# Kernel tuning notes

Hardware: AMD Instinct MI355X
Metric: run time of the kernel (lower is better)

Reference implementation:

```python
import jax, jax.numpy as jnp
import numpy as np

DG = 4      # deformable groups
KS = 3      # kernel size
PAD = (KS - 1) // 2


def _deform_conv2d(x, offset, weight, dg=DG, pad=PAD):
    """Deformable conv v1 (stride 1, dilation 1, same padding, no bias).
    x:      [B, Cin, H, W]
    offset: [B, dg*2*K, H, W], layout (g, k, {y,x}) in channel dim
    weight: [Cout, Cin, kh, kw]
    """
    B, Cin, H, W = x.shape
    Cout, _, kh, kw = weight.shape
    K = kh * kw
    Cg = Cin // dg
    off = offset.reshape(B, dg, K, 2, H, W)
    # kernel tap coordinates, flattened row-major
    ky = jnp.repeat(jnp.arange(kh), kw).astype(x.dtype)   # [K]
    kx = jnp.tile(jnp.arange(kw), kh).astype(x.dtype)     # [K]
    # sampling positions [B, dg, K, H, W]
    py = off[:, :, :, 0] + (jnp.arange(H, dtype=x.dtype)[None, None, None, :, None]
                            + ky[None, None, :, None, None] - pad)
    px = off[:, :, :, 1] + (jnp.arange(W, dtype=x.dtype)[None, None, None, None, :]
                            + kx[None, None, :, None, None] - pad)
    y0 = jnp.floor(py)
    x0 = jnp.floor(px)
    xg = x.reshape(B, dg, Cg, H * W)
    val = jnp.zeros((B, dg, Cg, K, H, W), x.dtype)
    for dy in (0.0, 1.0):
        for dx in (0.0, 1.0):
            yc = y0 + dy
            xc = x0 + dx
            w = (1.0 - jnp.abs(py - yc)) * (1.0 - jnp.abs(px - xc))
            valid = (yc >= 0) & (yc <= H - 1) & (xc >= 0) & (xc <= W - 1)
            w = jnp.where(valid, w, 0.0)                      # zero padding
            idx = (jnp.clip(yc, 0, H - 1).astype(jnp.int32) * W
                   + jnp.clip(xc, 0, W - 1).astype(jnp.int32))  # [B,dg,K,H,W]
            idx_b = jnp.broadcast_to(idx.reshape(B, dg, 1, K * H * W),
                                     (B, dg, Cg, K * H * W))
            g = jnp.take_along_axis(xg, idx_b, axis=3).reshape(B, dg, Cg, K, H, W)
            val = val + w[:, :, None] * g
    # grouped-offset but dense conv: contract over (dg, Cg, K)
    wk = weight.reshape(Cout, dg, Cg, K)
    return jnp.einsum('bgckhw,ogck->bohw', val, wk)


def setup_inputs() -> dict:
    key = jax.random.key(0)
    k1, k2, k3, k4, k5, k6 = jax.random.split(key, 6)
    B, C, H, W = 2, 256, 64, 64
    reg_feat = jax.random.normal(k1, (B, C, H, W), jnp.float32)
    cls_feat = jax.random.normal(k2, (B, C, H, W), jnp.float32)
    pred_init = jax.random.normal(k3, (B, 34, H, W), jnp.float32)
    w_offset = jax.random.normal(k4, (DG * 2 * KS * KS, 34), jnp.float32) * 0.1
    w_reg = jax.random.normal(k5, (C, C, KS, KS), jnp.float32) * 0.01
    w_cls = jax.random.normal(k6, (C, C, KS, KS), jnp.float32) * 0.01
    return {"reg_feat": reg_feat, "cls_feat": cls_feat, "pred_init": pred_init,
            "w_offset": w_offset, "w_reg": w_reg, "w_cls": w_cls}


def reference(reg_feat, cls_feat, pred_init, w_offset, w_reg, w_cls):
    # 1x1 conv (bias-free) predicting offsets from detached anchor predictions
    offset = jnp.einsum('oc,bchw->bohw', w_offset, jax.lax.stop_gradient(pred_init))
    reg_refine = jax.nn.relu(_deform_conv2d(reg_feat, offset, w_reg))
    cls_refine = jax.nn.relu(_deform_conv2d(cls_feat, offset, w_cls))
    return (reg_refine, cls_refine)
```

## Files before the change

kernel.cpp:

```cpp
#include <hip/hip_runtime.h>
#include <hip/hip_bf16.h>
#include <stdint.h>

#define HW   4096
#define NB   2

typedef float f32x4 __attribute__((ext_vector_type(4)));
typedef short s16x8 __attribute__((ext_vector_type(8)));

__device__ __forceinline__ unsigned short f2bf(float f) {
    union { float f; unsigned int u; } v; v.f = f;
    unsigned int u = v.u;
    unsigned int r = (u + 0x7FFFu + ((u >> 16) & 1u)) >> 16;
    return (unsigned short)r;
}

__device__ __forceinline__ float bf2f(unsigned short u) {
    union { unsigned int u; float f; } v; v.u = ((unsigned int)u) << 16;
    return v.f;
}

__global__ void __launch_bounds__(256)
k_prep(const float* __restrict__ pred, const float* __restrict__ wo,
       const float* __restrict__ regf, const float* __restrict__ clsf,
       const float* __restrict__ wr,   const float* __restrict__ wc,
       float4* __restrict__ wbuf, int4* __restrict__ ibuf,
       unsigned short* __restrict__ fbuf, unsigned short* __restrict__ wfrag) {
    int bb = blockIdx.x;
    if (bb < 1152) {
        int loc = bb * 256 + threadIdx.x;
        int p  = loc & 4095;
        int g  = (loc >> 12) & 3;
        int bk = loc >> 14;
        int b  = bk / 9;
        int k  = bk - b * 9;
        int rowy = ((g * 9 + k) * 2) * 34;
        float oy = 0.f, ox = 0.f;
        const float* pb = pred + (size_t)b * 34 * HW + p;
        #pragma unroll
        for (int c = 0; c < 34; ++c) {
            float pv = pb[c * HW];
            oy += wo[rowy + c]      * pv;
            ox += wo[rowy + 34 + c] * pv;
        }
        int h = p >> 6, w = p & 63;
        int ky = k / 3, kx = k - ky * 3;
        float py = oy + (float)(h + ky - 1);
        float px = ox + (float)(w + kx - 1);
        float fy0 = floorf(py), fx0 = floorf(px);
        int y0 = (int)fy0, x0 = (int)fx0;
        float fy = py - fy0, fx = px - fx0;
        float wy0 = 1.f - fy, wy1 = fy, wx0 = 1.f - fx, wx1 = fx;
        if (!(y0 >= 0  && y0 <= 63)) wy0 = 0.f;
        if (!(y0 >= -1 && y0 <= 62)) wy1 = 0.f;
        if (!(x0 >= 0  && x0 <= 63)) wx0 = 0.f;
        if (!(x0 >= -1 && x0 <= 62)) wx1 = 0.f;
        int cy0 = min(max(y0, 0), 63),     cy1 = min(max(y0 + 1, 0), 63);
        int cx0 = min(max(x0, 0), 63),     cx1 = min(max(x0 + 1, 0), 63);
        wbuf[loc] = make_float4(wy0 * wx0, wy0 * wx1, wy1 * wx0, wy1 * wx1);
        ibuf[loc] = make_int4((cy0 * 64 + cx0) << 9, (cy0 * 64 + cx1) << 9,
                              (cy1 * 64 + cx0) << 9, (cy1 * 64 + cx1) << 9);
    } else if (bb < 2176) {
        __shared__ float tile[64][65];
        int bid = bb - 1152;
        int pt = bid & 63;
        int cb = (bid >> 6) & 3;
        int b  = (bid >> 8) & 1;
        int cv = bid >> 9;
        const float* src = cv ? clsf : regf;
        int t = threadIdx.x;
        int pl = t & 63, q = t >> 6;
        #pragma unroll
        for (int i = 0; i < 16; ++i) {
            int cl = q + i * 4;
            tile[cl][pl] = src[((size_t)(b * 256 + cb * 64 + cl)) * HW + pt * 64 + pl];
        }
        __syncthreads();
        int cpair = t & 31, prow = t >> 5;
        #pragma unroll
        for (int i = 0; i < 8; ++i) {
            int p = i * 8 + prow;
            unsigned int u0 = f2bf(tile[cpair * 2][p]);
            unsigned int u1 = f2bf(tile[cpair * 2 + 1][p]);
            *(unsigned int*)&fbuf[((size_t)((cv * 2 + b) * HW + pt * 64 + p)) * 256
                                  + cb * 64 + cpair * 2] = u0 | (u1 << 16);
        }
    } else {
        int L = (bb - 2176) * 256 + threadIdx.x;
        int conv = L / 73728;
        int r = L - conv * 73728;
        int lane = r & 63;
        int ot = (r >> 6) & 15;
        int kk = (r >> 10) & 1;
        int s  = r >> 11;
        int k = s >> 2, g = s & 3;
        int o  = ot * 16 + (lane & 15);
        int cb = kk * 32 + (lane >> 4) * 8;
        const float* w = conv ? wc : wr;
        s16x8 v;
        #pragma unroll
        for (int j = 0; j < 8; ++j) {
            int c = cb + j;
            v[j] = (short)f2bf(w[((size_t)o * 256 + g * 64 + c) * 9 + k]);
        }
        *(s16x8*)(wfrag + (size_t)L * 8) = v;
    }
}

__global__ void __launch_bounds__(512, 2)
k_main(const float4* __restrict__ wbuf, const int4* __restrict__ ibuf,
       const unsigned short* __restrict__ fbuf, const unsigned short* __restrict__ wfrag,
       float* __restrict__ out) {
    __shared__ __align__(16) unsigned short vt[2][64][72];

    int bid0 = blockIdx.x;
    int bid = (bid0 & 7) * 32 + (bid0 >> 3);
    int conv = bid >> 7;
    int b    = (bid >> 6) & 1;
    int pt   = bid & 63;
    int p0   = pt * 64;

    int tid  = threadIdx.x;
    int lane = tid & 63;
    int wv   = tid >> 6;
    int px   = tid >> 3;
    int cg   = tid & 7;

    const char* fbb = (const char*)(fbuf + (size_t)(conv * 2 + b) * HW * 256);
    const unsigned short* wfc = wfrag + (size_t)conv * 73728 * 8;

    f32x4 acc[2][4];
    #pragma unroll
    for (int i = 0; i < 2; ++i)
        #pragma unroll
        for (int j = 0; j < 4; ++j)
            acc[i][j] = (f32x4){0.f, 0.f, 0.f, 0.f};

    struct Par { float4 w4; int4 io; };
    struct Gat { s16x8 a, b, c, d; };

    auto ldpar = [&](int s) -> Par {
        int k = s >> 2, g = s & 3;
        int pidx = ((b * 9 + k) * 4 + g) * HW + p0 + px;
        Par P; P.w4 = wbuf[pidx]; P.io = ibuf[pidx];
        return P;
    };

    auto gather = [&](const Par& P, int g) -> Gat {
        const char* base = fbb + g * 128 + cg * 16;
        Gat G;
        G.a = *(const s16x8*)(base + P.io.x);
        G.b = *(const s16x8*)(base + P.io.y);
        G.c = *(const s16x8*)(base + P.io.z);
        G.d = *(const s16x8*)(base + P.io.w);
        return G;
    };

    auto finish = [&](const Par& P, const Gat& G, int buf) {
        float r[8];
        #pragma unroll
        for (int j = 0; j < 8; ++j) {
            r[j] = P.w4.x * bf2f((unsigned short)G.a[j])
                 + P.w4.y * bf2f((unsigned short)G.b[j])
                 + P.w4.z * bf2f((unsigned short)G.c[j])
                 + P.w4.w * bf2f((unsigned short)G.d[j]);
        }
        s16x8 pk;
        #pragma unroll
        for (int j = 0; j < 8; ++j) pk[j] = (short)f2bf(r[j]);
        *(s16x8*)&vt[buf][px][cg * 8] = pk;
    };

    s16x8 af00, af01, af10, af11;
    auto loadA = [&](int s) {
        const unsigned short* wfs = wfc + (size_t)s * 2048 * 8;
        af00 = *(const s16x8*)(wfs + ((size_t)( 0 + wv * 2 + 0) * 64 + lane) * 8);
        af01 = *(const s16x8*)(wfs + ((size_t)( 0 + wv * 2 + 1) * 64 + lane) * 8);
        af10 = *(const s16x8*)(wfs + ((size_t)(16 + wv * 2 + 0) * 64 + lane) * 8);
        af11 = *(const s16x8*)(wfs + ((size_t)(16 + wv * 2 + 1) * 64 + lane) * 8);
    };

    auto domfma = [&](int s) {
        s16x8 bfr[4];
        #pragma unroll
        for (int np = 0; np < 4; ++np)
            bfr[np] = *(const s16x8*)
                &vt[s & 1][np * 16 + (lane & 15)][(lane >> 4) * 8];
        #pragma unroll
        for (int np = 0; np < 4; ++np)
            acc[0][np] = __builtin_amdgcn_mfma_f32_16x16x32_bf16(af00, bfr[np],
                                                                 acc[0][np], 0, 0, 0);
        #pragma unroll
        for (int np = 0; np < 4; ++np)
            acc[1][np] = __builtin_amdgcn_mfma_f32_16x16x32_bf16(af01, bfr[np],
                                                                 acc[1][np], 0, 0, 0);
        #pragma unroll
        for (int np = 0; np < 4; ++np)
            bfr[np] = *(const s16x8*)
                &vt[s & 1][np * 16 + (lane & 15)][32 + (lane >> 4) * 8];
        #pragma unroll
        for (int np = 0; np < 4; ++np)
            acc[0][np] = __builtin_amdgcn_mfma_f32_16x16x32_bf16(af10, bfr[np],
                                                                 acc[0][np], 0, 0, 0);
        #pragma unroll
        for (int np = 0; np < 4; ++np)
            acc[1][np] = __builtin_amdgcn_mfma_f32_16x16x32_bf16(af11, bfr[np],
                                                                 acc[1][np], 0, 0, 0);
    };

    loadA(0);
    Par P0 = ldpar(0);
    Gat G0 = gather(P0, 0);
    finish(P0, G0, 0);
    Par P1 = ldpar(1);
    Par P2 = ldpar(2);
    Gat G1 = gather(P1, 1);

    for (int s = 0; s < 36; ++s) {
        Gat Gn;
        Par Pn;
        if (s + 2 < 36) Gn = gather(P2, (s + 2) & 3);
        Pn = (s + 3 < 36) ? ldpar(s + 3) : P2;
        asm volatile("s_waitcnt lgkmcnt(0)" ::: "memory");
        __builtin_amdgcn_s_barrier();
        domfma(s);
        if (s + 1 < 36) {
            loadA(s + 1);
            finish(P1, G1, (s + 1) & 1);
        }
        P1 = P2; P2 = Pn; G1 = Gn;
    }

    float* ob = out + (size_t)conv * (NB * 256 * HW) + (size_t)b * 256 * HW;
    #pragma unroll
    for (int mo = 0; mo < 2; ++mo)
        #pragma unroll
        for (int np = 0; np < 4; ++np)
            #pragma unroll
            for (int r = 0; r < 4; ++r) {
                int o = wv * 32 + mo * 16 + (lane >> 4) * 4 + r;
                int p = p0 + np * 16 + (lane & 15);
                float v = acc[mo][np][r];
                ob[(size_t)o * HW + p] = v > 0.f ? v : 0.f;
            }
}

extern "C" void kernel_launch(void* const* d_in, const int* in_sizes, int n_in,
                              void* d_out, int out_size, void* d_ws, size_t ws_size,
                              hipStream_t stream) {
    (void)in_sizes; (void)n_in; (void)out_size; (void)ws_size;
    const float* reg_feat = (const float*)d_in[0];
    const float* cls_feat = (const float*)d_in[1];
    const float* pred     = (const float*)d_in[2];
    const float* w_off    = (const float*)d_in[3];
    const float* w_reg    = (const float*)d_in[4];
    const float* w_cls    = (const float*)d_in[5];
    float* out = (float*)d_out;
    char* ws = (char*)d_ws;
    float4*         wbuf  = (float4*)ws;
    int4*           ibuf  = (int4*)(ws + 4718592);
    unsigned short* fbuf  = (unsigned short*)(ws + 9437184);
    unsigned short* wfrag = (unsigned short*)(ws + 17825792);

    k_prep<<<2752, 256, 0, stream>>>(pred, w_off, reg_feat, cls_feat, w_reg, w_cls,
                                     wbuf, ibuf, fbuf, wfrag);
    k_main<<< 256, 512, 0, stream>>>(wbuf, ibuf, fbuf, wfrag, out);
}
```

Before: 53.22 us.

## Pack bilinear params to fp16/16-bit and double threads per block in main kernel

The bilinear weights and indices are packed into one int4 per sample, with fp16 weights and 16-bit pixel indices, halving the parameter buffer traffic. The main kernel now runs 1024 threads per block. Each thread gathers 4 channels instead of 8, and each wave computes 16 output channels instead of 32, which spreads the gather and MFMA work across more waves to hide latency. The cost is fp16 rounding of the interpolation weights, more waves synchronising at each barrier, and a doubled load of the per-pixel parameters, since 16 threads instead of 8 now read each pixel's entry.

```diff
diff --git a/kernel.cpp b/kernel.cpp
--- a/kernel.cpp
+++ b/kernel.cpp
@@ -7,6 +7,7 @@
 
 typedef float f32x4 __attribute__((ext_vector_type(4)));
 typedef short s16x8 __attribute__((ext_vector_type(8)));
+typedef short s16x4 __attribute__((ext_vector_type(4)));
 
 __device__ __forceinline__ unsigned short f2bf(float f) {
     union { float f; unsigned int u; } v; v.f = f;
@@ -20,11 +21,19 @@
     return v.f;
 }
 
+__device__ __forceinline__ unsigned int f2h(float f) {
+    union { _Float16 h; unsigned short u; } v; v.h = (_Float16)f; return v.u;
+}
+
+__device__ __forceinline__ float h2f(unsigned int u) {
+    union { unsigned short u; _Float16 h; } v; v.u = (unsigned short)u; return (float)v.h;
+}
+
 __global__ void __launch_bounds__(256)
 k_prep(const float* __restrict__ pred, const float* __restrict__ wo,
        const float* __restrict__ regf, const float* __restrict__ clsf,
        const float* __restrict__ wr,   const float* __restrict__ wc,
-       float4* __restrict__ wbuf, int4* __restrict__ ibuf,
+       int4* __restrict__ pbuf,
        unsigned short* __restrict__ fbuf, unsigned short* __restrict__ wfrag) {
     int bb = blockIdx.x;
     if (bb < 1152) {
@@ -57,9 +66,14 @@
         if (!(x0 >= -1 && x0 <= 62)) wx1 = 0.f;
         int cy0 = min(max(y0, 0), 63),     cy1 = min(max(y0 + 1, 0), 63);
         int cx0 = min(max(x0, 0), 63),     cx1 = min(max(x0 + 1, 0), 63);
-        wbuf[loc] = make_float4(wy0 * wx0, wy0 * wx1, wy1 * wx0, wy1 * wx1);
-        ibuf[loc] = make_int4((cy0 * 64 + cx0) << 9, (cy0 * 64 + cx1) << 9,
-                              (cy1 * 64 + cx0) << 9, (cy1 * 64 + cx1) << 9);
+        int r0 = cy0 * 64 + cx0, r1 = cy0 * 64 + cx1;
+        int r2 = cy1 * 64 + cx0, r3 = cy1 * 64 + cx1;
+        int4 pk;
+        pk.x = (int)(f2h(wy0 * wx0) | (f2h(wy0 * wx1) << 16));
+        pk.y = (int)(f2h(wy1 * wx0) | (f2h(wy1 * wx1) << 16));
+        pk.z = (int)((unsigned)r0 | ((unsigned)r1 << 16));
+        pk.w = (int)((unsigned)r2 | ((unsigned)r3 << 16));
+        pbuf[loc] = pk;
     } else if (bb < 2176) {
         __shared__ float tile[64][65];
         int bid = bb - 1152;
@@ -107,8 +121,8 @@
     }
 }
 
-__global__ void __launch_bounds__(512, 2)
-k_main(const float4* __restrict__ wbuf, const int4* __restrict__ ibuf,
+__global__ void __launch_bounds__(1024, 4)
+k_main(const int4* __restrict__ pbuf,
        const unsigned short* __restrict__ fbuf, const unsigned short* __restrict__ wfrag,
        float* __restrict__ out) {
     __shared__ __align__(16) unsigned short vt[2][64][72];
@@ -123,61 +137,58 @@
     int tid  = threadIdx.x;
     int lane = tid & 63;
     int wv   = tid >> 6;
-    int px   = tid >> 3;
-    int cg   = tid & 7;
-
-    const char* fbb = (const char*)(fbuf + (size_t)(conv * 2 + b) * HW * 256);
+    int px   = tid >> 4;
+    int cg   = tid & 15;
+
+    const char* fbb = (const char*)(fbuf + (size_t)(conv * 2 + b) * HW * 256) + cg * 8;
     const unsigned short* wfc = wfrag + (size_t)conv * 73728 * 8;
-
-    f32x4 acc[2][4];
+    const int4* pbb = pbuf + (size_t)b * 9 * 4 * HW + p0 + px;
+
+    f32x4 acc[4];
     #pragma unroll
-    for (int i = 0; i < 2; ++i)
-        #pragma unroll
-        for (int j = 0; j < 4; ++j)
-            acc[i][j] = (f32x4){0.f, 0.f, 0.f, 0.f};
-
-    struct Par { float4 w4; int4 io; };
-    struct Gat { s16x8 a, b, c, d; };
-
-    auto ldpar = [&](int s) -> Par {
+    for (int j = 0; j < 4; ++j) acc[j] = (f32x4){0.f, 0.f, 0.f, 0.f};
+
+    struct Gat { s16x4 a, b, c, d; };
+
+    auto ldpar = [&](int s) -> int4 {
         int k = s >> 2, g = s & 3;
-        int pidx = ((b * 9 + k) * 4 + g) * HW + p0 + px;
-        Par P; P.w4 = wbuf[pidx]; P.io = ibuf[pidx];
-        return P;
-    };
-
-    auto gather = [&](const Par& P, int g) -> Gat {
-        const char* base = fbb + g * 128 + cg * 16;
+        return pbb[(k * 4 + g) * HW];
+    };
+
+    auto gather = [&](const int4& P, int g) -> Gat {
+        const char* base = fbb + g * 128;
+        int o0 = ((unsigned)P.z & 0xffffu) << 9;
+        int o1 = ((unsigned)P.z >> 16) << 9;
+        int o2 = ((unsigned)P.w & 0xffffu) << 9;
+        int o3 = ((unsigned)P.w >> 16) << 9;
         Gat G;
-        G.a = *(const s16x8*)(base + P.io.x);
-        G.b = *(const s16x8*)(base + P.io.y);
-        G.c = *(const s16x8*)(base + P.io.z);
-        G.d = *(const s16x8*)(base + P.io.w);
+        G.a = *(const s16x4*)(base + o0);
+        G.b = *(const s16x4*)(base + o1);
+        G.c = *(const s16x4*)(base + o2);
+        G.d = *(const s16x4*)(base + o3);
         return G;
     };
 
-    auto finish = [&](const Par& P, const Gat& G, int buf) {
-        float r[8];
-        #pragma unroll
-        for (int j = 0; j < 8; ++j) {
-            r[j] = P.w4.x * bf2f((unsigned short)G.a[j])
-                 + P.w4.y * bf2f((unsigned short)G.b[j])
-                 + P.w4.z * bf2f((unsigned short)G.c[j])
-                 + P.w4.w * bf2f((unsigned short)G.d[j]);
-        }
-        s16x8 pk;
-        #pragma unroll
-        for (int j = 0; j < 8; ++j) pk[j] = (short)f2bf(r[j]);
-        *(s16x8*)&vt[buf][px][cg * 8] = pk;
-    };
-
-    s16x8 af00, af01, af10, af11;
+    auto finish = [&](const int4& P, const Gat& G, int buf) {
+        float w0 = h2f((unsigned)P.x & 0xffffu), w1 = h2f((unsigned)P.x >> 16);
+        float w2 = h2f((unsigned)P.y & 0xffffu), w3 = h2f((unsigned)P.y >> 16);
+        s16x4 pk;
+        #pragma unroll
+        for (int j = 0; j < 4; ++j) {
+            float r = w0 * bf2f((unsigned short)G.a[j])
+                    + w1 * bf2f((unsigned short)G.b[j])
+                    + w2 * bf2f((unsigned short)G.c[j])
+                    + w3 * bf2f((unsigned short)G.d[j]);
+            pk[j] = (short)f2bf(r);
+        }
+        *(s16x4*)&vt[buf][px][cg * 4] = pk;
+    };
+
+    s16x8 af0, af1;
     auto loadA = [&](int s) {
         const unsigned short* wfs = wfc + (size_t)s * 2048 * 8;
-        af00 = *(const s16x8*)(wfs + ((size_t)( 0 + wv * 2 + 0) * 64 + lane) * 8);
-        af01 = *(const s16x8*)(wfs + ((size_t)( 0 + wv * 2 + 1) * 64 + lane) * 8);
-        af10 = *(const s16x8*)(wfs + ((size_t)(16 + wv * 2 + 0) * 64 + lane) * 8);
-        af11 = *(const s16x8*)(wfs + ((size_t)(16 + wv * 2 + 1) * 64 + lane) * 8);
+        af0 = *(const s16x8*)(wfs + ((size_t)( 0 + wv) * 64 + lane) * 8);
+        af1 = *(const s16x8*)(wfs + ((size_t)(16 + wv) * 64 + lane) * 8);
     };
 
     auto domfma = [&](int s) {
@@ -188,37 +199,29 @@
                 &vt[s & 1][np * 16 + (lane & 15)][(lane >> 4) * 8];
         #pragma unroll
         for (int np = 0; np < 4; ++np)
-            acc[0][np] = __builtin_amdgcn_mfma_f32_16x16x32_bf16(af00, bfr[np],
-                                                                 acc[0][np], 0, 0, 0);
-        #pragma unroll
-        for (int np = 0; np < 4; ++np)
-            acc[1][np] = __builtin_amdgcn_mfma_f32_16x16x32_bf16(af01, bfr[np],
-                                                                 acc[1][np], 0, 0, 0);
+            acc[np] = __builtin_amdgcn_mfma_f32_16x16x32_bf16(af0, bfr[np],
+                                                              acc[np], 0, 0, 0);
         #pragma unroll
         for (int np = 0; np < 4; ++np)
             bfr[np] = *(const s16x8*)
                 &vt[s & 1][np * 16 + (lane & 15)][32 + (lane >> 4) * 8];
         #pragma unroll
         for (int np = 0; np < 4; ++np)
-            acc[0][np] = __builtin_amdgcn_mfma_f32_16x16x32_bf16(af10, bfr[np],
-                                                                 acc[0][np], 0, 0, 0);
-        #pragma unroll
-        for (int np = 0; np < 4; ++np)
-            acc[1][np] = __builtin_amdgcn_mfma_f32_16x16x32_bf16(af11, bfr[np],
-                                                                 acc[1][np], 0, 0, 0);
+            acc[np] = __builtin_amdgcn_mfma_f32_16x16x32_bf16(af1, bfr[np],
+                                                              acc[np], 0, 0, 0);
     };
 
     loadA(0);
-    Par P0 = ldpar(0);
+    int4 P0 = ldpar(0);
     Gat G0 = gather(P0, 0);
     finish(P0, G0, 0);
-    Par P1 = ldpar(1);
-    Par P2 = ldpar(2);
+    int4 P1 = ldpar(1);
+    int4 P2 = ldpar(2);
     Gat G1 = gather(P1, 1);
 
     for (int s = 0; s < 36; ++s) {
         Gat Gn;
-        Par Pn;
+        int4 Pn;
         if (s + 2 < 36) Gn = gather(P2, (s + 2) & 3);
         Pn = (s + 3 < 36) ? ldpar(s + 3) : P2;
         asm volatile("s_waitcnt lgkmcnt(0)" ::: "memory");
@@ -233,16 +236,14 @@
 
     float* ob = out + (size_t)conv * (NB * 256 * HW) + (size_t)b * 256 * HW;
     #pragma unroll
-    for (int mo = 0; mo < 2; ++mo)
-        #pragma unroll
-        for (int np = 0; np < 4; ++np)
-            #pragma unroll
-            for (int r = 0; r < 4; ++r) {
-                int o = wv * 32 + mo * 16 + (lane >> 4) * 4 + r;
-                int p = p0 + np * 16 + (lane & 15);
-                float v = acc[mo][np][r];
-                ob[(size_t)o * HW + p] = v > 0.f ? v : 0.f;
-            }
+    for (int np = 0; np < 4; ++np)
+        #pragma unroll
+        for (int r = 0; r < 4; ++r) {
+            int o = wv * 16 + (lane >> 4) * 4 + r;
+            int p = p0 + np * 16 + (lane & 15);
+            float v = acc[np][r];
+            ob[(size_t)o * HW + p] = v > 0.f ? v : 0.f;
+        }
 }
 
 extern "C" void kernel_launch(void* const* d_in, const int* in_sizes, int n_in,
@@ -257,12 +258,11 @@
     const float* w_cls    = (const float*)d_in[5];
     float* out = (float*)d_out;
     char* ws = (char*)d_ws;
-    float4*         wbuf  = (float4*)ws;
-    int4*           ibuf  = (int4*)(ws + 4718592);
-    unsigned short* fbuf  = (unsigned short*)(ws + 9437184);
-    unsigned short* wfrag = (unsigned short*)(ws + 17825792);
+    int4*           pbuf  = (int4*)ws;
+    unsigned short* fbuf  = (unsigned short*)(ws + 4718592);
+    unsigned short* wfrag = (unsigned short*)(ws + 13107200);
 
     k_prep<<<2752, 256, 0, stream>>>(pred, w_off, reg_feat, cls_feat, w_reg, w_cls,
-                                     wbuf, ibuf, fbuf, wfrag);
-    k_main<<< 256, 512, 0, stream>>>(wbuf, ibuf, fbuf, wfrag, out);
-}
+                                     pbuf, fbuf, wfrag);
+    k_main<<< 256, 1024, 0, stream>>>(pbuf, fbuf, wfrag, out);
+}
```

New measurement: 62.46 us. +17.4%, slower.
